# Kernel tuning notes

Measured on AMD Instinct MI355X. Metric: run time of the kernel, lower is better.

The kernel has to match this reference:

```python
import jax, jax.numpy as jnp
import numpy as np

N = 50000
E = 500000
HID = 128
H = 4
D = HID // H
NUM_EDGE_TYPES = 8
EPS_LN = 1e-5


def setup_inputs() -> dict:
    key = jax.random.key(0)
    ks = jax.random.split(key, 16)
    s = 1.0 / np.sqrt(HID)
    return {
        "node_embeddings": jax.random.normal(ks[0], (N, HID), jnp.float32),
        "edge_index": jax.random.randint(ks[1], (2, E), 0, N, jnp.int32),
        "edge_type": jax.random.randint(ks[2], (E,), 0, NUM_EDGE_TYPES, jnp.int32),
        "task_embedding": jax.random.normal(ks[3], (HID,), jnp.float32),
        "W_src": jax.random.normal(ks[4], (HID, HID), jnp.float32) * s,
        "b_src": jnp.zeros((HID,), jnp.float32),
        "W_dst": jax.random.normal(ks[5], (HID, HID), jnp.float32) * s,
        "b_dst": jnp.zeros((HID,), jnp.float32),
        "edge_emb": jax.random.normal(ks[6], (NUM_EDGE_TYPES, HID), jnp.float32),
        "att": jax.random.normal(ks[7], (H, D), jnp.float32) * s,
        "W_out": jax.random.normal(ks[8], (HID, HID), jnp.float32) * s,
        "b_out": jnp.zeros((HID,), jnp.float32),
        "norm_w": jnp.ones((HID,), jnp.float32),
        "norm_b": jnp.zeros((HID,), jnp.float32),
        "W_film": jax.random.normal(ks[9], (HID, 2 * HID), jnp.float32) * s,
        "b_film": jnp.zeros((2 * HID,), jnp.float32),
    }


def reference(node_embeddings, edge_index, edge_type, task_embedding,
              W_src, b_src, W_dst, b_dst, edge_emb, att,
              W_out, b_out, norm_w, norm_b, W_film, b_film):
    num_nodes = node_embeddings.shape[0]
    src, dst = edge_index[0], edge_index[1]

    # Node projections -> [N, H, D]
    x_src = (node_embeddings @ W_src + b_src).reshape(num_nodes, H, D)
    x_dst = (node_embeddings @ W_dst + b_dst).reshape(num_nodes, H, D)
    e = edge_emb[edge_type].reshape(-1, H, D)  # [E, H, D]

    # GATv2 attention logits per edge per head
    combined = jax.nn.leaky_relu(x_src[src] + x_dst[dst] + e, negative_slope=0.2)
    logits = jnp.einsum('ehd,hd->eh', combined, att)  # [E, H]

    # Scatter-softmax over destination nodes
    mx = jax.ops.segment_max(logits, dst, num_segments=num_nodes)  # [N, H]
    mx = jnp.where(jnp.isinf(mx), jnp.zeros_like(mx), mx)
    ex = jnp.exp(logits - mx[dst])
    sums = jax.ops.segment_sum(ex, dst, num_segments=num_nodes)  # [N, H]
    attn = ex / jnp.maximum(sums[dst], 1e-12)  # [E, H]

    # Weighted message aggregation
    msg = x_src[src] * attn[..., None]  # [E, H, D]
    agg = jax.ops.segment_sum(msg, dst, num_segments=num_nodes)  # [N, H, D]
    agg = agg.reshape(num_nodes, HID) @ W_out + b_out

    # Task FiLM modulation
    film = task_embedding @ W_film + b_film  # [2*HID]
    gamma, beta = film[:HID], film[HID:]
    agg = agg * (1.0 + 0.5 * jnp.tanh(gamma))[None, :] + beta[None, :]

    # Residual + LayerNorm
    y = node_embeddings + agg
    mu = jnp.mean(y, axis=-1, keepdims=True)
    var = jnp.mean((y - mu) ** 2, axis=-1, keepdims=True)
    return (y - mu) / jnp.sqrt(var + EPS_LN) * norm_w + norm_b
```

## Files before the change

### kernel.cpp

```cpp
#include <hip/hip_runtime.h>
#include <hip/hip_bf16.h>

#define N_NODES 50000
#define E_EDGES 500000
#define HID 128
#define NHEAD 4
#define HDIM 32
#define SCAN_BLOCKS ((N_NODES + 255) / 256)

__global__ __launch_bounds__(256) void film_kernel(
    const float* __restrict__ task, const float* __restrict__ Wf,
    const float* __restrict__ bf, float* __restrict__ film)
{
    __shared__ float tsk[HID];
    const int t = threadIdx.x;
    if (t < HID) tsk[t] = task[t];
    __syncthreads();
    float acc = bf[t];
    #pragma unroll 8
    for (int k = 0; k < HID; ++k)
        acc = fmaf(tsk[k], Wf[k * 256 + t], acc);
    if (t < HID) film[t] = 1.f + 0.5f * tanhf(acc);
    else         film[t] = acc;
}

__global__ __launch_bounds__(256) void gemm_srcdst(
    const float* __restrict__ A,
    const float* __restrict__ Ws, const float* __restrict__ bs,
    const float* __restrict__ Wd, const float* __restrict__ bd,
    float* __restrict__ xs, float* __restrict__ xd)
{
    __shared__ float a_tile[64][HID];
    const int t  = threadIdx.x;
    const int nb = blockIdx.x * 64;

    #pragma unroll
    for (int i = 0; i < 8; ++i) {
        int f  = t + 256 * i;
        int m  = f >> 5;
        int k4 = f & 31;
        int node = nb + m;
        float4 v;
        if (node < N_NODES) v = *(const float4*)(A + (size_t)node * HID + k4 * 4);
        else { v.x = v.y = v.z = v.w = 0.f; }
        *(float4*)&a_tile[m][k4 * 4] = v;
    }
    __syncthreads();

    const int wave = t >> 6;
    const int lane = t & 63;
    const bool is_src = (wave < 2);
    const int cc = (lane & 31) * 4;
    const int m0 = (wave & 1) * 32 + (lane >> 5) * 16;
    const float* W    = is_src ? Ws : Wd;
    const float* bias = is_src ? bs : bd;
    float*       xout = is_src ? xs : xd;

    float acc[16][4];
    #pragma unroll
    for (int m = 0; m < 16; ++m)
        #pragma unroll
        for (int j = 0; j < 4; ++j) acc[m][j] = 0.f;

    for (int kc = 0; kc < 32; ++kc) {
        const int k0 = kc * 4;
        const float4 w0 = *(const float4*)(W + (size_t)(k0 + 0) * HID + cc);
        const float4 w1 = *(const float4*)(W + (size_t)(k0 + 1) * HID + cc);
        const float4 w2 = *(const float4*)(W + (size_t)(k0 + 2) * HID + cc);
        const float4 w3 = *(const float4*)(W + (size_t)(k0 + 3) * HID + cc);
        #pragma unroll
        for (int m = 0; m < 16; ++m) {
            const float4 av = *(const float4*)&a_tile[m0 + m][k0];
            acc[m][0] = fmaf(av.x, w0.x, acc[m][0]);
            acc[m][1] = fmaf(av.x, w0.y, acc[m][1]);
            acc[m][2] = fmaf(av.x, w0.z, acc[m][2]);
            acc[m][3] = fmaf(av.x, w0.w, acc[m][3]);
            acc[m][0] = fmaf(av.y, w1.x, acc[m][0]);
            acc[m][1] = fmaf(av.y, w1.y, acc[m][1]);
            acc[m][2] = fmaf(av.y, w1.z, acc[m][2]);
            acc[m][3] = fmaf(av.y, w1.w, acc[m][3]);
            acc[m][0] = fmaf(av.z, w2.x, acc[m][0]);
            acc[m][1] = fmaf(av.z, w2.y, acc[m][1]);
            acc[m][2] = fmaf(av.z, w2.z, acc[m][2]);
            acc[m][3] = fmaf(av.z, w2.w, acc[m][3]);
            acc[m][0] = fmaf(av.w, w3.x, acc[m][0]);
            acc[m][1] = fmaf(av.w, w3.y, acc[m][1]);
            acc[m][2] = fmaf(av.w, w3.z, acc[m][2]);
            acc[m][3] = fmaf(av.w, w3.w, acc[m][3]);
        }
    }

    const float4 bv = *(const float4*)(bias + cc);
    #pragma unroll
    for (int m = 0; m < 16; ++m) {
        const int node = nb + m0 + m;
        if (node < N_NODES) {
            float4 o;
            o.x = acc[m][0] + bv.x;
            o.y = acc[m][1] + bv.y;
            o.z = acc[m][2] + bv.z;
            o.w = acc[m][3] + bv.w;
            *(float4*)(xout + (size_t)node * HID + cc) = o;
        }
    }
}

__global__ __launch_bounds__(256) void hist_kernel(
    const int* __restrict__ ei, int* __restrict__ deg)
{
    const int e = blockIdx.x * 256 + threadIdx.x;
    if (e < E_EDGES) atomicAdd(&deg[ei[E_EDGES + e]], 1);
}

__global__ __launch_bounds__(256) void reduce_blocks(
    const int* __restrict__ deg, int* __restrict__ blocksum)
{
    __shared__ int ws_[4];
    const int t = threadIdx.x;
    const int i = blockIdx.x * 256 + t;
    int v = (i < N_NODES) ? deg[i] : 0;
    #pragma unroll
    for (int off = 32; off; off >>= 1) v += __shfl_down(v, off);
    if ((t & 63) == 0) ws_[t >> 6] = v;
    __syncthreads();
    if (t == 0) blocksum[blockIdx.x] = ws_[0] + ws_[1] + ws_[2] + ws_[3];
}

__global__ __launch_bounds__(256) void scan_blocksums(
    const int* __restrict__ blocksum, int* __restrict__ blockoff,
    int* __restrict__ rowptr)
{
    __shared__ int wtot[4];
    const int t    = threadIdx.x;
    const int lane = t & 63;
    const int w    = t >> 6;
    int v = (t < SCAN_BLOCKS) ? blocksum[t] : 0;
    const int own = v;
    #pragma unroll
    for (int off = 1; off < 64; off <<= 1) {
        const int u = __shfl_up(v, off);
        if (lane >= off) v += u;
    }
    if (lane == 63) wtot[w] = v;
    __syncthreads();
    int woff = 0;
    #pragma unroll
    for (int k = 0; k < 4; ++k) if (k < w) woff += wtot[k];
    if (t < SCAN_BLOCKS) blockoff[t] = woff + v - own;
    if (t == 0) rowptr[N_NODES] = E_EDGES;
}

__global__ __launch_bounds__(256) void scan_within(
    const int* __restrict__ deg, const int* __restrict__ blockoff,
    int* __restrict__ rowptr, int* __restrict__ cursor)
{
    __shared__ int wtot[4];
    const int t    = threadIdx.x;
    const int lane = t & 63;
    const int w    = t >> 6;
    const int i    = blockIdx.x * 256 + t;
    int v = (i < N_NODES) ? deg[i] : 0;
    const int own = v;
    #pragma unroll
    for (int off = 1; off < 64; off <<= 1) {
        const int u = __shfl_up(v, off);
        if (lane >= off) v += u;
    }
    if (lane == 63) wtot[w] = v;
    __syncthreads();
    int woff = blockoff[blockIdx.x];
    #pragma unroll
    for (int k = 0; k < 4; ++k) if (k < w) woff += wtot[k];
    if (i < N_NODES) {
        const int ex = woff + v - own;
        rowptr[i] = ex;
        cursor[i] = ex;
    }
}

__global__ __launch_bounds__(256) void scatter_kernel(
    const int* __restrict__ ei, const int* __restrict__ et,
    int* __restrict__ cursor, int* __restrict__ pack)
{
    const int e = blockIdx.x * 256 + threadIdx.x;
    if (e < E_EDGES) {
        const int d = ei[E_EDGES + e];
        const int pos = atomicAdd(&cursor[d], 1);
        pack[pos] = ei[e] | (et[e] << 16);
    }
}

__global__ __launch_bounds__(256) void gather_agg(
    const int* __restrict__ rowptr, const int* __restrict__ pack,
    const float* __restrict__ xsrc, const float* __restrict__ xdst,
    const float* __restrict__ eemb, const float* __restrict__ att,
    float* __restrict__ agg)
{
    const int lane = threadIdx.x & 31;
    const int grp  = threadIdx.x >> 5;
    const int node = blockIdx.x * 8 + grp;
    if (node >= N_NODES) return;

    const float4 av = *(const float4*)(att + lane * 4);
    const float4 xd = *(const float4*)(xdst + (size_t)node * HID + lane * 4);

    float a0 = 0.f, a1 = 0.f, a2 = 0.f, a3 = 0.f, sum = 0.f;
    const int b = rowptr[node];
    const int e = rowptr[node + 1];

    int i = b;
    for (; i + 1 < e; i += 2) {
        const int pk0 = pack[i];
        const int pk1 = pack[i + 1];
        const int s0 = pk0 & 0xFFFF, ty0 = pk0 >> 16;
        const int s1 = pk1 & 0xFFFF, ty1 = pk1 >> 16;
        const float4 xs0 = *(const float4*)(xsrc + (size_t)s0 * HID + lane * 4);
        const float4 ev0 = *(const float4*)(eemb + (size_t)ty0 * HID + lane * 4);
        const float4 xs1 = *(const float4*)(xsrc + (size_t)s1 * HID + lane * 4);
        const float4 ev1 = *(const float4*)(eemb + (size_t)ty1 * HID + lane * 4);
        float c, p0 = 0.f, p1 = 0.f;
        c = xs0.x + xd.x + ev0.x; c = (c > 0.f) ? c : 0.2f * c; p0 = fmaf(c, av.x, p0);
        c = xs0.y + xd.y + ev0.y; c = (c > 0.f) ? c : 0.2f * c; p0 = fmaf(c, av.y, p0);
        c = xs0.z + xd.z + ev0.z; c = (c > 0.f) ? c : 0.2f * c; p0 = fmaf(c, av.z, p0);
        c = xs0.w + xd.w + ev0.w; c = (c > 0.f) ? c : 0.2f * c; p0 = fmaf(c, av.w, p0);
        c = xs1.x + xd.x + ev1.x; c = (c > 0.f) ? c : 0.2f * c; p1 = fmaf(c, av.x, p1);
        c = xs1.y + xd.y + ev1.y; c = (c > 0.f) ? c : 0.2f * c; p1 = fmaf(c, av.y, p1);
        c = xs1.z + xd.z + ev1.z; c = (c > 0.f) ? c : 0.2f * c; p1 = fmaf(c, av.z, p1);
        c = xs1.w + xd.w + ev1.w; c = (c > 0.f) ? c : 0.2f * c; p1 = fmaf(c, av.w, p1);
        p0 += __shfl_xor(p0, 1); p1 += __shfl_xor(p1, 1);
        p0 += __shfl_xor(p0, 2); p1 += __shfl_xor(p1, 2);
        p0 += __shfl_xor(p0, 4); p1 += __shfl_xor(p1, 4);
        const float ex0 = expf(p0);
        const float ex1 = expf(p1);
        a0 = fmaf(ex0, xs0.x, a0); a1 = fmaf(ex0, xs0.y, a1);
        a2 = fmaf(ex0, xs0.z, a2); a3 = fmaf(ex0, xs0.w, a3);
        a0 = fmaf(ex1, xs1.x, a0); a1 = fmaf(ex1, xs1.y, a1);
        a2 = fmaf(ex1, xs1.z, a2); a3 = fmaf(ex1, xs1.w, a3);
        sum += ex0 + ex1;
    }
    if (i < e) {
        const int pk0 = pack[i];
        const int s0 = pk0 & 0xFFFF, ty0 = pk0 >> 16;
        const float4 xs0 = *(const float4*)(xsrc + (size_t)s0 * HID + lane * 4);
        const float4 ev0 = *(const float4*)(eemb + (size_t)ty0 * HID + lane * 4);
        float c, p0 = 0.f;
        c = xs0.x + xd.x + ev0.x; c = (c > 0.f) ? c : 0.2f * c; p0 = fmaf(c, av.x, p0);
        c = xs0.y + xd.y + ev0.y; c = (c > 0.f) ? c : 0.2f * c; p0 = fmaf(c, av.y, p0);
        c = xs0.z + xd.z + ev0.z; c = (c > 0.f) ? c : 0.2f * c; p0 = fmaf(c, av.z, p0);
        c = xs0.w + xd.w + ev0.w; c = (c > 0.f) ? c : 0.2f * c; p0 = fmaf(c, av.w, p0);
        p0 += __shfl_xor(p0, 1);
        p0 += __shfl_xor(p0, 2);
        p0 += __shfl_xor(p0, 4);
        const float ex0 = expf(p0);
        a0 = fmaf(ex0, xs0.x, a0); a1 = fmaf(ex0, xs0.y, a1);
        a2 = fmaf(ex0, xs0.z, a2); a3 = fmaf(ex0, xs0.w, a3);
        sum += ex0;
    }

    const float inv = 1.f / fmaxf(sum, 1e-12f);
    float4 o;
    o.x = a0 * inv; o.y = a1 * inv; o.z = a2 * inv; o.w = a3 * inv;
    *(float4*)(agg + (size_t)node * HID + lane * 4) = o;
}

__global__ __launch_bounds__(256) void finalize(
    const float* __restrict__ agg,
    const float* __restrict__ A,   const float* __restrict__ Wo,
    const float* __restrict__ bo,  const float* __restrict__ film,
    const float* __restrict__ nw_, const float* __restrict__ nb_,
    float* __restrict__ out)
{
    __shared__ float a_tile[64][HID];
    const int t  = threadIdx.x;
    const int nb = blockIdx.x * 64;

    #pragma unroll
    for (int i = 0; i < 8; ++i) {
        int f  = t + 256 * i;
        int m  = f >> 5;
        int k4 = f & 31;
        int node = nb + m;
        float4 v;
        if (node < N_NODES) v = *(const float4*)(agg + (size_t)node * HID + k4 * 4);
        else { v.x = v.y = v.z = v.w = 0.f; }
        *(float4*)&a_tile[m][k4 * 4] = v;
    }
    __syncthreads();

    const int cg = t & 31;
    const int rg = t >> 5;
    const int cc = cg * 4;
    const int m0 = rg * 8;

    float acc[8][4];
    #pragma unroll
    for (int m = 0; m < 8; ++m)
        #pragma unroll
        for (int j = 0; j < 4; ++j) acc[m][j] = 0.f;

    for (int kc = 0; kc < 32; ++kc) {
        const int k0 = kc * 4;
        const float4 w0 = *(const float4*)(Wo + (size_t)(k0 + 0) * HID + cc);
        const float4 w1 = *(const float4*)(Wo + (size_t)(k0 + 1) * HID + cc);
        const float4 w2 = *(const float4*)(Wo + (size_t)(k0 + 2) * HID + cc);
        const float4 w3 = *(const float4*)(Wo + (size_t)(k0 + 3) * HID + cc);
        #pragma unroll
        for (int m = 0; m < 8; ++m) {
            const float4 av = *(const float4*)&a_tile[m0 + m][k0];
            acc[m][0] = fmaf(av.x, w0.x, acc[m][0]);
            acc[m][1] = fmaf(av.x, w0.y, acc[m][1]);
            acc[m][2] = fmaf(av.x, w0.z, acc[m][2]);
            acc[m][3] = fmaf(av.x, w0.w, acc[m][3]);
            acc[m][0] = fmaf(av.y, w1.x, acc[m][0]);
            acc[m][1] = fmaf(av.y, w1.y, acc[m][1]);
            acc[m][2] = fmaf(av.y, w1.z, acc[m][2]);
            acc[m][3] = fmaf(av.y, w1.w, acc[m][3]);
            acc[m][0] = fmaf(av.z, w2.x, acc[m][0]);
            acc[m][1] = fmaf(av.z, w2.y, acc[m][1]);
            acc[m][2] = fmaf(av.z, w2.z, acc[m][2]);
            acc[m][3] = fmaf(av.z, w2.w, acc[m][3]);
            acc[m][0] = fmaf(av.w, w3.x, acc[m][0]);
            acc[m][1] = fmaf(av.w, w3.y, acc[m][1]);
            acc[m][2] = fmaf(av.w, w3.z, acc[m][2]);
            acc[m][3] = fmaf(av.w, w3.w, acc[m][3]);
        }
    }

    const float4 bv  = *(const float4*)(bo   + cc);
    const float4 gfv = *(const float4*)(film + cc);
    const float4 btv = *(const float4*)(film + HID + cc);
    const float4 nwv = *(const float4*)(nw_  + cc);
    const float4 nbv = *(const float4*)(nb_  + cc);

    #pragma unroll
    for (int m = 0; m < 8; ++m) {
        const int node = nb + m0 + m;
        float4 y;
        float4 r;
        if (node < N_NODES) r = *(const float4*)(A + (size_t)node * HID + cc);
        else { r.x = r.y = r.z = r.w = 0.f; }
        y.x = fmaf(acc[m][0] + bv.x, gfv.x, btv.x) + r.x;
        y.y = fmaf(acc[m][1] + bv.y, gfv.y, btv.y) + r.y;
        y.z = fmaf(acc[m][2] + bv.z, gfv.z, btv.z) + r.z;
        y.w = fmaf(acc[m][3] + bv.w, gfv.w, btv.w) + r.w;

        float s1 = y.x + y.y + y.z + y.w;
        float s2 = y.x * y.x + y.y * y.y + y.z * y.z + y.w * y.w;
        #pragma unroll
        for (int off = 1; off < 32; off <<= 1) {
            s1 += __shfl_xor(s1, off);
            s2 += __shfl_xor(s2, off);
        }
        const float mu   = s1 * (1.f / 128.f);
        const float var  = s2 * (1.f / 128.f) - mu * mu;
        const float rsig = rsqrtf(var + 1e-5f);
        if (node < N_NODES) {
            float4 o;
            o.x = (y.x - mu) * rsig * nwv.x + nbv.x;
            o.y = (y.y - mu) * rsig * nwv.y + nbv.y;
            o.z = (y.z - mu) * rsig * nwv.z + nbv.z;
            o.w = (y.w - mu) * rsig * nwv.w + nbv.w;
            *(float4*)(out + (size_t)node * HID + cc) = o;
        }
    }
}

extern "C" void kernel_launch(void* const* d_in, const int* in_sizes, int n_in,
                              void* d_out, int out_size, void* d_ws, size_t ws_size,
                              hipStream_t stream)
{
    const float* node_emb = (const float*)d_in[0];
    const int*   edge_idx = (const int*)  d_in[1];
    const int*   edge_ty  = (const int*)  d_in[2];
    const float* task     = (const float*)d_in[3];
    const float* W_src    = (const float*)d_in[4];
    const float* b_src    = (const float*)d_in[5];
    const float* W_dst    = (const float*)d_in[6];
    const float* b_dst    = (const float*)d_in[7];
    const float* edge_emb = (const float*)d_in[8];
    const float* att      = (const float*)d_in[9];
    const float* W_out    = (const float*)d_in[10];
    const float* b_out    = (const float*)d_in[11];
    const float* norm_w   = (const float*)d_in[12];
    const float* norm_b   = (const float*)d_in[13];
    const float* W_film   = (const float*)d_in[14];
    const float* b_film   = (const float*)d_in[15];
    float* out = (float*)d_out;

    char* ws = (char*)d_ws;
    float* x_src    = (float*)ws;                            ws += (size_t)N_NODES * HID * 4;
    float* x_dst    = (float*)ws;                            ws += (size_t)N_NODES * HID * 4;
    float* agg      = (float*)ws;                            ws += (size_t)N_NODES * HID * 4;
    float* film     = (float*)ws;                            ws += 256 * 4;
    int*   deg      = (int*)ws;                              ws += (size_t)N_NODES * 4;
    int*   rowptr   = (int*)ws;                              ws += (size_t)(N_NODES + 1) * 4;
    int*   cursor   = (int*)ws;                              ws += (size_t)N_NODES * 4;
    int*   blocksum = (int*)ws;                              ws += 256 * 4;
    int*   blockoff = (int*)ws;                              ws += 256 * 4;
    int*   pack     = (int*)ws;                              ws += (size_t)E_EDGES * 4;

    hipMemsetAsync(deg, 0, (size_t)N_NODES * sizeof(int), stream);

    film_kernel<<<1, 256, 0, stream>>>(task, W_film, b_film, film);
    hist_kernel<<<(E_EDGES + 255) / 256, 256, 0, stream>>>(edge_idx, deg);
    gemm_srcdst<<<(N_NODES + 63) / 64, 256, 0, stream>>>(
        node_emb, W_src, b_src, W_dst, b_dst, x_src, x_dst);
    reduce_blocks<<<SCAN_BLOCKS, 256, 0, stream>>>(deg, blocksum);
    scan_blocksums<<<1, 256, 0, stream>>>(blocksum, blockoff, rowptr);
    scan_within<<<SCAN_BLOCKS, 256, 0, stream>>>(deg, blockoff, rowptr, cursor);
    scatter_kernel<<<(E_EDGES + 255) / 256, 256, 0, stream>>>(
        edge_idx, edge_ty, cursor, pack);
    gather_agg<<<(N_NODES + 7) / 8, 256, 0, stream>>>(
        rowptr, pack, x_src, x_dst, edge_emb, att, agg);
    finalize<<<(N_NODES + 63) / 64, 256, 0, stream>>>(
        agg, node_emb, W_out, b_out, film, norm_w, norm_b, out);
}
```

Before: 296.9 us.

## Use bf16 MFMA for src/dst projections and store projections as bf16

```diff
diff --git a/kernel.cpp b/kernel.cpp
--- a/kernel.cpp
+++ b/kernel.cpp
@@ -8,6 +8,18 @@
 #define HDIM 32
 #define SCAN_BLOCKS ((N_NODES + 255) / 256)
 
+typedef __attribute__((ext_vector_type(8))) short bf16x8;
+typedef __attribute__((ext_vector_type(4))) float f32x4;
+
+static __device__ __forceinline__ float b2f(unsigned short u) {
+    return __uint_as_float((unsigned int)u << 16);
+}
+static __device__ __forceinline__ unsigned short f2b(float f) {
+    unsigned int u = __float_as_uint(f);
+    u += 0x7FFFu + ((u >> 16) & 1u);
+    return (unsigned short)(u >> 16);
+}
+
 __global__ __launch_bounds__(256) void film_kernel(
     const float* __restrict__ task, const float* __restrict__ Wf,
     const float* __restrict__ bf, float* __restrict__ film)
@@ -24,83 +36,80 @@
     else         film[t] = acc;
 }
 
-__global__ __launch_bounds__(256) void gemm_srcdst(
-    const float* __restrict__ A,
-    const float* __restrict__ Ws, const float* __restrict__ bs,
-    const float* __restrict__ Wd, const float* __restrict__ bd,
-    float* __restrict__ xs, float* __restrict__ xd)
-{
-    __shared__ float a_tile[64][HID];
+__global__ __launch_bounds__(256) void prep_weights(
+    const float* __restrict__ Ws, const float* __restrict__ Wd,
+    short* __restrict__ B1)
+{
+    const int id = blockIdx.x * 256 + threadIdx.x;
+    const int n = id >> 7;
+    const int k = id & 127;
+    const float v = (n < HID) ? Ws[(size_t)k * HID + n]
+                              : Wd[(size_t)k * HID + (n - HID)];
+    B1[(size_t)n * HID + k] = (short)f2b(v);
+}
+
+__global__ __launch_bounds__(256) void gemm_mfma(
+    const float* __restrict__ A, const short* __restrict__ B1,
+    const float* __restrict__ bs, const float* __restrict__ bd,
+    unsigned short* __restrict__ xs, unsigned short* __restrict__ xd)
+{
+    __shared__ unsigned short a_lds[64 * HID];
     const int t  = threadIdx.x;
     const int nb = blockIdx.x * 64;
 
     #pragma unroll
     for (int i = 0; i < 8; ++i) {
-        int f  = t + 256 * i;
-        int m  = f >> 5;
-        int k4 = f & 31;
-        int node = nb + m;
+        const int f   = t + 256 * i;
+        const int row = f >> 5;
+        const int k4  = f & 31;
+        const int node = nb + row;
         float4 v;
         if (node < N_NODES) v = *(const float4*)(A + (size_t)node * HID + k4 * 4);
         else { v.x = v.y = v.z = v.w = 0.f; }
-        *(float4*)&a_tile[m][k4 * 4] = v;
-    }
-    __syncthreads();
-
-    const int wave = t >> 6;
-    const int lane = t & 63;
-    const bool is_src = (wave < 2);
-    const int cc = (lane & 31) * 4;
-    const int m0 = (wave & 1) * 32 + (lane >> 5) * 16;
-    const float* W    = is_src ? Ws : Wd;
-    const float* bias = is_src ? bs : bd;
-    float*       xout = is_src ? xs : xd;
-
-    float acc[16][4];
-    #pragma unroll
-    for (int m = 0; m < 16; ++m)
+        ushort4 h;
+        h.x = f2b(v.x); h.y = f2b(v.y); h.z = f2b(v.z); h.w = f2b(v.w);
+        int byte = row * 256 + k4 * 8;
+        byte ^= (row & 7) << 4;
+        *(ushort4*)((char*)a_lds + byte) = h;
+    }
+    __syncthreads();
+
+    const int w   = t >> 6;
+    const int l   = t & 63;
+    const int l15 = l & 15;
+    const int kg  = l >> 4;
+    const int r   = w * 16 + l15;
+
+    f32x4 acc[16];
+    #pragma unroll
+    for (int nf = 0; nf < 16; ++nf) acc[nf] = (f32x4){0.f, 0.f, 0.f, 0.f};
+
+    #pragma unroll
+    for (int ks = 0; ks < 4; ++ks) {
+        int abyte = r * 256 + ks * 64 + kg * 16;
+        abyte ^= (r & 7) << 4;
+        const bf16x8 a = *(const bf16x8*)((char*)a_lds + abyte);
         #pragma unroll
-        for (int j = 0; j < 4; ++j) acc[m][j] = 0.f;
-
-    for (int kc = 0; kc < 32; ++kc) {
-        const int k0 = kc * 4;
-        const float4 w0 = *(const float4*)(W + (size_t)(k0 + 0) * HID + cc);
-        const float4 w1 = *(const float4*)(W + (size_t)(k0 + 1) * HID + cc);
-        const float4 w2 = *(const float4*)(W + (size_t)(k0 + 2) * HID + cc);
-        const float4 w3 = *(const float4*)(W + (size_t)(k0 + 3) * HID + cc);
+        for (int nf = 0; nf < 16; ++nf) {
+            const bf16x8 b = *(const bf16x8*)(
+                B1 + (size_t)(nf * 16 + l15) * HID + ks * 32 + kg * 8);
+            acc[nf] = __builtin_amdgcn_mfma_f32_16x16x32_bf16(a, b, acc[nf], 0, 0, 0);
+        }
+    }
+
+    #pragma unroll
+    for (int nf = 0; nf < 16; ++nf) {
+        const int col = nf * 16 + l15;
+        const bool is_src = (col < HID);
+        const float bias = is_src ? bs[col] : bd[col - HID];
         #pragma unroll
-        for (int m = 0; m < 16; ++m) {
-            const float4 av = *(const float4*)&a_tile[m0 + m][k0];
-            acc[m][0] = fmaf(av.x, w0.x, acc[m][0]);
-            acc[m][1] = fmaf(av.x, w0.y, acc[m][1]);
-            acc[m][2] = fmaf(av.x, w0.z, acc[m][2]);
-            acc[m][3] = fmaf(av.x, w0.w, acc[m][3]);
-            acc[m][0] = fmaf(av.y, w1.x, acc[m][0]);
-            acc[m][1] = fmaf(av.y, w1.y, acc[m][1]);
-            acc[m][2] = fmaf(av.y, w1.z, acc[m][2]);
-            acc[m][3] = fmaf(av.y, w1.w, acc[m][3]);
-            acc[m][0] = fmaf(av.z, w2.x, acc[m][0]);
-            acc[m][1] = fmaf(av.z, w2.y, acc[m][1]);
-            acc[m][2] = fmaf(av.z, w2.z, acc[m][2]);
-            acc[m][3] = fmaf(av.z, w2.w, acc[m][3]);
-            acc[m][0] = fmaf(av.w, w3.x, acc[m][0]);
-            acc[m][1] = fmaf(av.w, w3.y, acc[m][1]);
-            acc[m][2] = fmaf(av.w, w3.z, acc[m][2]);
-            acc[m][3] = fmaf(av.w, w3.w, acc[m][3]);
-        }
-    }
-
-    const float4 bv = *(const float4*)(bias + cc);
-    #pragma unroll
-    for (int m = 0; m < 16; ++m) {
-        const int node = nb + m0 + m;
-        if (node < N_NODES) {
-            float4 o;
-            o.x = acc[m][0] + bv.x;
-            o.y = acc[m][1] + bv.y;
-            o.z = acc[m][2] + bv.z;
-            o.w = acc[m][3] + bv.w;
-            *(float4*)(xout + (size_t)node * HID + cc) = o;
+        for (int j = 0; j < 4; ++j) {
+            const int node = nb + w * 16 + kg * 4 + j;
+            if (node < N_NODES) {
+                const unsigned short us = f2b(acc[nf][j] + bias);
+                if (is_src) xs[(size_t)node * HID + col] = us;
+                else        xd[(size_t)node * HID + (col - HID)] = us;
+            }
         }
     }
 }
@@ -192,7 +201,8 @@
 
 __global__ __launch_bounds__(256) void gather_agg(
     const int* __restrict__ rowptr, const int* __restrict__ pack,
-    const float* __restrict__ xsrc, const float* __restrict__ xdst,
+    const unsigned short* __restrict__ xsrc,
+    const unsigned short* __restrict__ xdst,
     const float* __restrict__ eemb, const float* __restrict__ att,
     float* __restrict__ agg)
 {
@@ -202,7 +212,9 @@
     if (node >= N_NODES) return;
 
     const float4 av = *(const float4*)(att + lane * 4);
-    const float4 xd = *(const float4*)(xdst + (size_t)node * HID + lane * 4);
+    const ushort4 xdu = *(const ushort4*)(xdst + (size_t)node * HID + lane * 4);
+    const float xdx = b2f(xdu.x), xdy = b2f(xdu.y),
+                xdz = b2f(xdu.z), xdw = b2f(xdu.w);
 
     float a0 = 0.f, a1 = 0.f, a2 = 0.f, a3 = 0.f, sum = 0.f;
     const int b = rowptr[node];
@@ -214,46 +226,49 @@
         const int pk1 = pack[i + 1];
         const int s0 = pk0 & 0xFFFF, ty0 = pk0 >> 16;
         const int s1 = pk1 & 0xFFFF, ty1 = pk1 >> 16;
-        const float4 xs0 = *(const float4*)(xsrc + (size_t)s0 * HID + lane * 4);
-        const float4 ev0 = *(const float4*)(eemb + (size_t)ty0 * HID + lane * 4);
-        const float4 xs1 = *(const float4*)(xsrc + (size_t)s1 * HID + lane * 4);
-        const float4 ev1 = *(const float4*)(eemb + (size_t)ty1 * HID + lane * 4);
+        const ushort4 u0 = *(const ushort4*)(xsrc + (size_t)s0 * HID + lane * 4);
+        const float4  ev0 = *(const float4*)(eemb + (size_t)ty0 * HID + lane * 4);
+        const ushort4 u1 = *(const ushort4*)(xsrc + (size_t)s1 * HID + lane * 4);
+        const float4  ev1 = *(const float4*)(eemb + (size_t)ty1 * HID + lane * 4);
+        const float x0x = b2f(u0.x), x0y = b2f(u0.y), x0z = b2f(u0.z), x0w = b2f(u0.w);
+        const float x1x = b2f(u1.x), x1y = b2f(u1.y), x1z = b2f(u1.z), x1w = b2f(u1.w);
         float c, p0 = 0.f, p1 = 0.f;
-        c = xs0.x + xd.x + ev0.x; c = (c > 0.f) ? c : 0.2f * c; p0 = fmaf(c, av.x, p0);
-        c = xs0.y + xd.y + ev0.y; c = (c > 0.f) ? c : 0.2f * c; p0 = fmaf(c, av.y, p0);
-        c = xs0.z + xd.z + ev0.z; c = (c > 0.f) ? c : 0.2f * c; p0 = fmaf(c, av.z, p0);
-        c = xs0.w + xd.w + ev0.w; c = (c > 0.f) ? c : 0.2f * c; p0 = fmaf(c, av.w, p0);
-        c = xs1.x + xd.x + ev1.x; c = (c > 0.f) ? c : 0.2f * c; p1 = fmaf(c, av.x, p1);
-        c = xs1.y + xd.y + ev1.y; c = (c > 0.f) ? c : 0.2f * c; p1 = fmaf(c, av.y, p1);
-        c = xs1.z + xd.z + ev1.z; c = (c > 0.f) ? c : 0.2f * c; p1 = fmaf(c, av.z, p1);
-        c = xs1.w + xd.w + ev1.w; c = (c > 0.f) ? c : 0.2f * c; p1 = fmaf(c, av.w, p1);
+        c = x0x + xdx + ev0.x; c = (c > 0.f) ? c : 0.2f * c; p0 = fmaf(c, av.x, p0);
+        c = x0y + xdy + ev0.y; c = (c > 0.f) ? c : 0.2f * c; p0 = fmaf(c, av.y, p0);
+        c = x0z + xdz + ev0.z; c = (c > 0.f) ? c : 0.2f * c; p0 = fmaf(c, av.z, p0);
+        c = x0w + xdw + ev0.w; c = (c > 0.f) ? c : 0.2f * c; p0 = fmaf(c, av.w, p0);
+        c = x1x + xdx + ev1.x; c = (c > 0.f) ? c : 0.2f * c; p1 = fmaf(c, av.x, p1);
+        c = x1y + xdy + ev1.y; c = (c > 0.f) ? c : 0.2f * c; p1 = fmaf(c, av.y, p1);
+        c = x1z + xdz + ev1.z; c = (c > 0.f) ? c : 0.2f * c; p1 = fmaf(c, av.z, p1);
+        c = x1w + xdw + ev1.w; c = (c > 0.f) ? c : 0.2f * c; p1 = fmaf(c, av.w, p1);
         p0 += __shfl_xor(p0, 1); p1 += __shfl_xor(p1, 1);
         p0 += __shfl_xor(p0, 2); p1 += __shfl_xor(p1, 2);
         p0 += __shfl_xor(p0, 4); p1 += __shfl_xor(p1, 4);
         const float ex0 = expf(p0);
         const float ex1 = expf(p1);
-        a0 = fmaf(ex0, xs0.x, a0); a1 = fmaf(ex0, xs0.y, a1);
-        a2 = fmaf(ex0, xs0.z, a2); a3 = fmaf(ex0, xs0.w, a3);
-        a0 = fmaf(ex1, xs1.x, a0); a1 = fmaf(ex1, xs1.y, a1);
-        a2 = fmaf(ex1, xs1.z, a2); a3 = fmaf(ex1, xs1.w, a3);
+        a0 = fmaf(ex0, x0x, a0); a1 = fmaf(ex0, x0y, a1);
+        a2 = fmaf(ex0, x0z, a2); a3 = fmaf(ex0, x0w, a3);
+        a0 = fmaf(ex1, x1x, a0); a1 = fmaf(ex1, x1y, a1);
+        a2 = fmaf(ex1, x1z, a2); a3 = fmaf(ex1, x1w, a3);
         sum += ex0 + ex1;
     }
     if (i < e) {
         const int pk0 = pack[i];
         const int s0 = pk0 & 0xFFFF, ty0 = pk0 >> 16;
-        const float4 xs0 = *(const float4*)(xsrc + (size_t)s0 * HID + lane * 4);
-        const float4 ev0 = *(const float4*)(eemb + (size_t)ty0 * HID + lane * 4);
+        const ushort4 u0 = *(const ushort4*)(xsrc + (size_t)s0 * HID + lane * 4);
+        const float4  ev0 = *(const float4*)(eemb + (size_t)ty0 * HID + lane * 4);
+        const float x0x = b2f(u0.x), x0y = b2f(u0.y), x0z = b2f(u0.z), x0w = b2f(u0.w);
         float c, p0 = 0.f;
-        c = xs0.x + xd.x + ev0.x; c = (c > 0.f) ? c : 0.2f * c; p0 = fmaf(c, av.x, p0);
-        c = xs0.y + xd.y + ev0.y; c = (c > 0.f) ? c : 0.2f * c; p0 = fmaf(c, av.y, p0);
-        c = xs0.z + xd.z + ev0.z; c = (c > 0.f) ? c : 0.2f * c; p0 = fmaf(c, av.z, p0);
-        c = xs0.w + xd.w + ev0.w; c = (c > 0.f) ? c : 0.2f * c; p0 = fmaf(c, av.w, p0);
+        c = x0x + xdx + ev0.x; c = (c > 0.f) ? c : 0.2f * c; p0 = fmaf(c, av.x, p0);
+        c = x0y + xdy + ev0.y; c = (c > 0.f) ? c : 0.2f * c; p0 = fmaf(c, av.y, p0);
+        c = x0z + xdz + ev0.z; c = (c > 0.f) ? c : 0.2f * c; p0 = fmaf(c, av.z, p0);
+        c = x0w + xdw + ev0.w; c = (c > 0.f) ? c : 0.2f * c; p0 = fmaf(c, av.w, p0);
         p0 += __shfl_xor(p0, 1);
         p0 += __shfl_xor(p0, 2);
         p0 += __shfl_xor(p0, 4);
         const float ex0 = expf(p0);
-        a0 = fmaf(ex0, xs0.x, a0); a1 = fmaf(ex0, xs0.y, a1);
-        a2 = fmaf(ex0, xs0.z, a2); a3 = fmaf(ex0, xs0.w, a3);
+        a0 = fmaf(ex0, x0x, a0); a1 = fmaf(ex0, x0y, a1);
+        a2 = fmaf(ex0, x0z, a2); a3 = fmaf(ex0, x0w, a3);
         sum += ex0;
     }
 
@@ -388,8 +403,6 @@
     float* out = (float*)d_out;
 
     char* ws = (char*)d_ws;
-    float* x_src    = (float*)ws;                            ws += (size_t)N_NODES * HID * 4;
-    float* x_dst    = (float*)ws;                            ws += (size_t)N_NODES * HID * 4;
     float* agg      = (float*)ws;                            ws += (size_t)N_NODES * HID * 4;
     float* film     = (float*)ws;                            ws += 256 * 4;
     int*   deg      = (int*)ws;                              ws += (size_t)N_NODES * 4;
@@ -398,13 +411,17 @@
     int*   blocksum = (int*)ws;                              ws += 256 * 4;
     int*   blockoff = (int*)ws;                              ws += 256 * 4;
     int*   pack     = (int*)ws;                              ws += (size_t)E_EDGES * 4;
+    unsigned short* x_src = (unsigned short*)ws;             ws += (size_t)N_NODES * HID * 2;
+    unsigned short* x_dst = (unsigned short*)ws;             ws += (size_t)N_NODES * HID * 2;
+    short* wb1      = (short*)ws;                            ws += (size_t)256 * HID * 2;
 
     hipMemsetAsync(deg, 0, (size_t)N_NODES * sizeof(int), stream);
 
     film_kernel<<<1, 256, 0, stream>>>(task, W_film, b_film, film);
     hist_kernel<<<(E_EDGES + 255) / 256, 256, 0, stream>>>(edge_idx, deg);
-    gemm_srcdst<<<(N_NODES + 63) / 64, 256, 0, stream>>>(
-        node_emb, W_src, b_src, W_dst, b_dst, x_src, x_dst);
+    prep_weights<<<(256 * HID) / 256, 256, 0, stream>>>(W_src, W_dst, wb1);
+    gemm_mfma<<<(N_NODES + 63) / 64, 256, 0, stream>>>(
+        node_emb, wb1, b_src, b_dst, x_src, x_dst);
     reduce_blocks<<<SCAN_BLOCKS, 256, 0, stream>>>(deg, blocksum);
     scan_blocksums<<<1, 256, 0, stream>>>(blocksum, blockoff, rowptr);
     scan_within<<<SCAN_BLOCKS, 256, 0, stream>>>(deg, blockoff, rowptr, cursor);
```

Result: faster. 290.0 us (-2.3%).
